# Performance work log

Hardware: AMD Instinct MI355X
Metric: run time of the kernel (lower is better)

Reference implementation:

```python
import jax, jax.numpy as jnp
import numpy as np

B, SEQ, H = 256, 200, 256
NFFT, HOP = 16, 8
FREQ = NFFT // 2 + 1          # 9
NSEG = SEQ // HOP + 1         # 26 (SEQ % HOP == 0 -> pad_len == 0)
FACTOR = 2


def _gelu(x):
    return jax.nn.gelu(x, approximate=False)  # torch nn.GELU / F.gelu default = exact erf


def _layernorm(x, w, b, eps=1e-12):
    u = x.mean(-1, keepdims=True)
    s = ((x - u) ** 2).mean(-1, keepdims=True)
    return w * (x - u) / jnp.sqrt(s + eps) + b


def _mixer(xr, xi, w1, b1, w2, b2):
    # complex MLP: einsum '...ijk,jkl->...ijl' with per-kept-dim weights
    e = lambda a, w: jnp.einsum('bijk,jkl->bijl', a, w)
    o1r = _gelu(e(xr, w1[0]) - e(xi, w1[1]) + b1[0])
    o1i = _gelu(e(xi, w1[0]) + e(xr, w1[1]) + b1[1])
    o2r = e(o1r, w2[0]) - e(o1i, w2[1]) + b2[0]
    # NOTE: faithful to the source bug: o1_image used in BOTH terms of o2_image
    o2i = e(o1i, w2[0]) + e(o1i, w2[1]) + b2[1]
    return o2r, o2i


def _stft(x):
    # torch.stft(n_fft=NFFT, hop=HOP, center=True, onesided=True, normalized=True,
    #            pad_mode='constant', window=None -> rectangular ones)
    pad = NFFT // 2
    xp = jnp.pad(x, ((0, 0), (pad, pad)))
    idx = jnp.arange(NSEG)[:, None] * HOP + jnp.arange(NFFT)[None, :]
    frames = xp[:, idx]                                    # [N, NSEG, NFFT]
    spec = jnp.fft.rfft(frames, axis=-1) * (NFFT ** -0.5)  # normalized=True
    return jnp.swapaxes(spec, -1, -2)                      # [N, FREQ, NSEG]


def _istft(spec):
    # torch.istft(center=True, normalized=True, rectangular window)
    n = spec.shape[0]
    frames = jnp.fft.irfft(jnp.swapaxes(spec, -1, -2) * (NFFT ** 0.5), n=NFFT, axis=-1)
    L = (NSEG - 1) * HOP + NFFT
    idx = (jnp.arange(NSEG)[:, None] * HOP + jnp.arange(NFFT)[None, :]).ravel()
    y = jnp.zeros((n, L), frames.dtype).at[:, idx].add(frames.reshape(n, -1))
    env = jnp.zeros((L,), frames.dtype).at[idx].add(1.0)   # window**2 overlap-add
    pad = NFFT // 2
    out_len = (NSEG - 1) * HOP                              # = SEQ
    return y[:, pad:pad + out_len] / env[pad:pad + out_len]


def setup_inputs() -> dict:
    key = jax.random.key(0)
    ks = jax.random.split(key, 24)
    p = lambda k, sh: jax.random.normal(k, sh, jnp.float32) * 0.02
    d = {}
    d["input_tensor"] = jax.random.normal(ks[0], (B, SEQ, H), jnp.float32)
    # grouped conv2d: weight [NSEG, 1, H, FREQ] -> stored as [NSEG, H, FREQ]
    d["conv_w"] = p(ks[1], (NSEG, H, FREQ)); d["conv_b"] = p(ks[2], (NSEG,))
    d["fm_w1"] = p(ks[3], (2, NSEG, FREQ, FREQ * FACTOR)); d["fm_b1"] = p(ks[4], (2, NSEG, FREQ * FACTOR))
    d["fm_w2"] = p(ks[5], (2, NSEG, FREQ * FACTOR, FREQ)); d["fm_b2"] = p(ks[6], (2, NSEG, FREQ))
    d["cm_w1"] = p(ks[7], (2, NSEG, H, H * FACTOR)); d["cm_b1"] = p(ks[8], (2, NSEG, H * FACTOR))
    d["cm_w2"] = p(ks[9], (2, NSEG, H * FACTOR, H)); d["cm_b2"] = p(ks[10], (2, NSEG, H))
    d["sm_w1"] = p(ks[11], (2, FREQ, NSEG, NSEG * FACTOR)); d["sm_b1"] = p(ks[12], (2, FREQ, NSEG * FACTOR))
    d["sm_w2"] = p(ks[13], (2, FREQ, NSEG * FACTOR, NSEG)); d["sm_b2"] = p(ks[14], (2, FREQ, NSEG))
    d["ln_w"] = jnp.ones((H,), jnp.float32); d["ln_b"] = jnp.zeros((H,), jnp.float32)
    d["ff_w1"] = p(ks[15], (H, 4 * H)); d["ff_b1"] = p(ks[16], (4 * H,))
    d["ff_w2"] = p(ks[17], (4 * H, H)); d["ff_b2"] = p(ks[18], (H,))
    d["ff_ln_w"] = jnp.ones((H,), jnp.float32); d["ff_ln_b"] = jnp.zeros((H,), jnp.float32)
    return d


def reference(input_tensor, conv_w, conv_b, fm_w1, fm_b1, fm_w2, fm_b2,
              cm_w1, cm_b1, cm_w2, cm_b2, sm_w1, sm_b1, sm_w2, sm_b2,
              ln_w, ln_b, ff_w1, ff_b1, ff_w2, ff_b2, ff_ln_w, ff_ln_b):
    b, seq, h = input_tensor.shape
    x = jnp.swapaxes(input_tensor, -1, -2).reshape(b * h, seq)  # pad_len == 0
    spec = _stft(x).reshape(b, h, FREQ, NSEG)
    xr, xi = spec.real, spec.imag
    xnorm = jnp.sqrt(xr ** 2 + xi ** 2)                         # [b,h,F,S]
    # grouped conv2d with full (H,FREQ) kernel == per-segment weighted sum
    w = jnp.einsum('bhfs,shf->bs', xnorm, conv_w) + conv_b
    w = w + jnp.exp(jnp.arange(1 - NSEG, 1, dtype=jnp.float32))  # exp decay bias
    xr = xr * w[:, None, None, :]
    xi = xi * w[:, None, None, :]
    # -> [b,h,S,F]: frequency mixing (kept=segment, mixed=freq)
    xr = jnp.swapaxes(xr, -1, -2); xi = jnp.swapaxes(xi, -1, -2)
    xr, xi = _mixer(xr, xi, fm_w1, fm_b1, fm_w2, fm_b2)
    # -> [b,F,S,h]: channel mixing (kept=segment, mixed=hidden)
    xr = jnp.swapaxes(xr, 1, 3); xi = jnp.swapaxes(xi, 1, 3)
    xr, xi = _mixer(xr, xi, cm_w1, cm_b1, cm_w2, cm_b2)
    # -> [b,h,F,S]: segment mixing (kept=freq, mixed=segment)
    xr = jnp.transpose(xr, (0, 3, 1, 2)); xi = jnp.transpose(xi, (0, 3, 1, 2))
    xr, xi = _mixer(xr, xi, sm_w1, sm_b1, sm_w2, sm_b2)
    spec = (xr + 1j * xi).reshape(b * h, FREQ, NSEG)
    y = _istft(spec)[:, :seq].reshape(b, h, seq)
    y = jnp.swapaxes(y, -1, -2)                                  # [b,seq,h]
    hs = _layernorm(y + input_tensor, ln_w, ln_b)                # dropout p=0
    ff = _gelu(hs @ ff_w1 + ff_b1) @ ff_w2 + ff_b2
    return _layernorm(ff + hs, ff_ln_w, ff_ln_b)
```

## Files before the change

kernel.cpp:

```cpp
#include <hip/hip_runtime.h>
#include <hip/hip_bf16.h>
#include <math.h>

typedef __hip_bfloat16 bf16;
typedef short bf16x8 __attribute__((ext_vector_type(8)));
typedef float f32x4 __attribute__((ext_vector_type(4)));

#define B_    256
#define SEQ_  200
#define H_    256
#define FREQ_ 9
#define NSEG_ 26
#define LDS64 64

__device__ __forceinline__ float ldb(const bf16* p, size_t i){ return __bfloat162float(p[i]); }
__device__ __forceinline__ void stb(bf16* p, size_t i, float v){ p[i] = __float2bfloat16(v); }
__device__ __forceinline__ short f2b(float v){ union{bf16 b; short s;} c; c.b = __float2bfloat16(v); return c.s; }
__device__ __forceinline__ unsigned short f2bu(float v){ union{bf16 b; unsigned short s;} c; c.b = __float2bfloat16(v); return c.s; }
__device__ __forceinline__ float gelu_(float x){
  float y  = 0.7978845608f*(x + 0.044715f*x*x*x);
  float ay = fabsf(y);
  float e  = __expf(-2.f*ay);
  float th = 1.f - 2.f*e*__builtin_amdgcn_rcpf(1.f + e);
  th = copysignf(th, y);
  return 0.5f*x*(1.f + th);
}

__device__ __constant__ float CT16[16] = {
  1.0f, 0.9238795325f, 0.7071067812f, 0.3826834324f, 0.0f, -0.3826834324f, -0.7071067812f, -0.9238795325f,
 -1.0f,-0.9238795325f,-0.7071067812f,-0.3826834324f, 0.0f,  0.3826834324f, 0.7071067812f,  0.9238795325f};
__device__ __constant__ float ST16[16] = {
  0.0f, 0.3826834324f, 0.7071067812f, 0.9238795325f, 1.0f,  0.9238795325f, 0.7071067812f,  0.3826834324f,
  0.0f,-0.3826834324f,-0.7071067812f,-0.9238795325f,-1.0f, -0.9238795325f,-0.7071067812f, -0.3826834324f};

__device__ __forceinline__ void gload16(const short* g, short* l){
  __builtin_amdgcn_global_load_lds(
      (const __attribute__((address_space(1))) unsigned int*)(const void*)g,
      (__attribute__((address_space(3))) unsigned int*)(void*)l, 16, 0, 0);
}

template<int ROWS>
__device__ __forceinline__ void stage_tile(short* lds, const short* src, int rstride, int tid){
  int rl = tid >> 3;
  int c  = tid & 7;
  #pragma unroll
  for(int p=0; p<ROWS/32; p++){
    int r = p*32 + rl;
    int csrc = c ^ (r & 7);
    gload16(src + (size_t)r*rstride + csrc*8, lds + r*LDS64 + c*8);
  }
}

__device__ __forceinline__ void mma_bk64(const short* lA, const short* lB, int wm, int wn,
                                         int lane, f32x4 acc[4][4]){
  int m_l = lane & 15, quad = lane >> 4;
  int sw = m_l & 7;
  #pragma unroll
  for(int ks=0; ks<64; ks+=32){
    int cs = (((ks>>3) + quad) ^ sw) * 8;
    bf16x8 a[4], b[4];
    #pragma unroll
    for(int i=0;i<4;i++) a[i] = *(const bf16x8*)&lA[(wm + i*16 + m_l)*LDS64 + cs];
    #pragma unroll
    for(int j=0;j<4;j++) b[j] = *(const bf16x8*)&lB[(wn + j*16 + m_l)*LDS64 + cs];
    #pragma unroll
    for(int i=0;i<4;i++)
      #pragma unroll
      for(int j=0;j<4;j++)
        acc[i][j] = __builtin_amdgcn_mfma_f32_16x16x32_bf16(a[i], b[j], acc[i][j], 0,0,0);
  }
}

__global__ __launch_bounds__(256) void k_prep_b1(const float* __restrict__ w1, short* __restrict__ B1t){
  int g = blockIdx.x;
  int jt = g & 7, ht = (g>>3)&3, p = (g>>5)&1, s = g>>6;
  __shared__ float tile[64][65];
  int t = threadIdx.x;
  const float* src = w1 + (size_t)p*3407872 + (size_t)s*131072;
  #pragma unroll
  for(int q=0;q<16;q++){
    int r = q*4 + (t>>6), c = t & 63;
    tile[r][c] = src[(size_t)(ht*64 + r)*512 + jt*64 + c];
  }
  __syncthreads();
  int n_l = t >> 2, kc = (t & 3)*16;
  short tA[16] __attribute__((aligned(16)));
  short tB[16] __attribute__((aligned(16)));
  #pragma unroll
  for(int i=0;i<16;i++){
    float v = tile[kc+i][n_l];
    tA[i] = (p==0) ? f2b(v) : f2b(-v);
    tB[i] = f2b(v);
  }
  int j = jt*64 + n_l, h = ht*64 + kc;
  size_t d1, d2;
  if(p==0){ d1 = ((size_t)(s*1024 + j))*512 + h;
            d2 = ((size_t)(s*1024 + 512 + j))*512 + 256 + h; }
  else    { d1 = ((size_t)(s*1024 + j))*512 + 256 + h;
            d2 = ((size_t)(s*1024 + 512 + j))*512 + h; }
  *(int4*)&B1t[d1] = *(int4*)&tA[0]; *(int4*)&B1t[d1+8] = *(int4*)&tA[8];
  *(int4*)&B1t[d2] = *(int4*)&tB[0]; *(int4*)&B1t[d2+8] = *(int4*)&tB[8];
}

__global__ __launch_bounds__(256) void k_prep_b2(const float* __restrict__ w2,
                                                 short* __restrict__ B2r, short* __restrict__ B2i){
  int g = blockIdx.x;
  int ht = g & 3, jt = (g>>2)&7, s = g>>5;
  __shared__ float t0[64][65], t1[64][65];
  int t = threadIdx.x;
  const float* s0 = w2 + (size_t)s*131072;
  const float* s1 = w2 + 3407872 + (size_t)s*131072;
  #pragma unroll
  for(int q=0;q<16;q++){
    int r = q*4 + (t>>6), c = t & 63;
    t0[r][c] = s0[(size_t)(jt*64 + r)*256 + ht*64 + c];
    t1[r][c] = s1[(size_t)(jt*64 + r)*256 + ht*64 + c];
  }
  __syncthreads();
  int n_l = t >> 2, jc = (t & 3)*16;
  short ta[16] __attribute__((aligned(16)));
  short tb[16] __attribute__((aligned(16)));
  short tc[16] __attribute__((aligned(16)));
  #pragma unroll
  for(int i=0;i<16;i++){
    float v0 = t0[jc+i][n_l], v1 = t1[jc+i][n_l];
    ta[i] = f2b(v0); tb[i] = f2b(-v1); tc[i] = f2b(v0+v1);
  }
  int n = ht*64 + n_l, j = jt*64 + jc;
  size_t dr = ((size_t)(s*256 + n))*1024 + j;
  size_t di = ((size_t)(s*256 + n))*512 + j;
  *(int4*)&B2r[dr]     = *(int4*)&ta[0]; *(int4*)&B2r[dr+8]     = *(int4*)&ta[8];
  *(int4*)&B2r[dr+512] = *(int4*)&tb[0]; *(int4*)&B2r[dr+520]   = *(int4*)&tb[8];
  *(int4*)&B2i[di]     = *(int4*)&tc[0]; *(int4*)&B2i[di+8]     = *(int4*)&tc[8];
}

__global__ __launch_bounds__(256) void k_transp(const float* __restrict__ src, short* __restrict__ dst,
                                                int R, int C){
  int ct = blockIdx.x % (C/64);
  int rt = blockIdx.x / (C/64);
  __shared__ float tile[64][65];
  int t = threadIdx.x;
  #pragma unroll
  for(int p=0;p<16;p++){
    int r = p*4 + (t>>6), c = t & 63;
    tile[r][c] = src[(size_t)(rt*64 + r)*C + ct*64 + c];
  }
  __syncthreads();
  int row_out = t >> 2, rc = (t & 3)*16;
  short tmp[16] __attribute__((aligned(16)));
  #pragma unroll
  for(int i=0;i<16;i++) tmp[i] = f2b(tile[rc+i][row_out]);
  size_t base = (size_t)(ct*64 + row_out)*R + rt*64 + rc;
  *(int4*)&dst[base] = *(int4*)&tmp[0]; *(int4*)&dst[base+8] = *(int4*)&tmp[8];
}

__global__ __launch_bounds__(256) void k_prep_sm(const float* __restrict__ w1, const float* __restrict__ w2,
                                                 short* __restrict__ B1sm, short* __restrict__ B2sm){
  int f = blockIdx.x;
  int t = threadIdx.x;
  for(int idx=t; idx<8192; idx+=256){
    int jp = idx >> 6, k = idx & 63;
    float v = 0.f;
    if(jp < 104){
      int j = (jp < 52) ? jp : jp - 52;
      if(k < 26){
        int s = k;
        v = (jp < 52) ? w1[f*1352 + s*52 + j] : w1[12168 + f*1352 + s*52 + j];
      } else if(k >= 32 && k < 58){
        int s = k - 32;
        v = (jp < 52) ? -w1[12168 + f*1352 + s*52 + j] : w1[f*1352 + s*52 + j];
      }
    }
    B1sm[(size_t)f*8192 + idx] = f2b(v);
  }
  for(int idx=t; idx<8192; idx+=256){
    int sop = idx >> 7, k = idx & 127;
    float v = 0.f;
    if(sop < 26){
      if(k < 52)       v = w2[f*1352 + k*26 + sop];
      else if(k < 104) v = -w2[12168 + f*1352 + (k-52)*26 + sop];
    } else if(sop < 52){
      int so = sop - 26;
      if(k >= 52 && k < 104)
        v = w2[f*1352 + (k-52)*26 + so] + w2[12168 + f*1352 + (k-52)*26 + so];
    }
    B2sm[(size_t)f*8192 + idx] = f2b(v);
  }
}

__global__ __launch_bounds__(256) void k_prep_fm(const float* __restrict__ w1, const float* __restrict__ w2,
                                                 short* __restrict__ B1fm, short* __restrict__ B2fm){
  int s = blockIdx.x;
  int t = threadIdx.x;
  for(int idx=t; idx<1536; idx+=256){
    int n = idx >> 5, k = idx & 31;
    float v = 0.f;
    if(n < 18){
      if(k < 9)       v = w1[s*162 + k*18 + n];
      else if(k < 18) v = -w1[4212 + s*162 + (k-9)*18 + n];
    } else if(n < 36){
      int j = n - 18;
      if(k < 9)       v = w1[4212 + s*162 + k*18 + j];
      else if(k < 18) v = w1[s*162 + (k-9)*18 + j];
    }
    B1fm[s*1536 + idx] = f2b(v);
  }
  for(int idx=t; idx<2048; idx+=256){
    int n = idx >> 6, k = idx & 63;
    float v = 0.f;
    if(n < 9){
      if(k < 18)      v = w2[s*162 + k*9 + n];
      else if(k < 36) v = -w2[4212 + s*162 + (k-18)*9 + n];
    } else if(n < 18){
      int f = n - 9;
      if(k >= 18 && k < 36)
        v = w2[s*162 + (k-18)*9 + f] + w2[4212 + s*162 + (k-18)*9 + f];
    }
    B2fm[s*2048 + idx] = f2b(v);
  }
}

__global__ __launch_bounds__(256) void k_prep_cw(const float* __restrict__ cw, float* __restrict__ cwT){
  int s = blockIdx.x; int t = threadIdx.x;
  __shared__ float tile[2304];
  for(int i=t; i<2304; i+=256) tile[i] = cw[s*2304 + i];
  __syncthreads();
  #pragma unroll
  for(int f=0; f<9; f++) cwT[(s*9+f)*256 + t] = tile[t*9+f];
}

#define LX1 40
#define LG1 72
__global__ __launch_bounds__(256) void k_sfm2(const float* __restrict__ inp,
                                              const float* __restrict__ cwT, const float* __restrict__ cb,
                                              const short* __restrict__ B1fm, const short* __restrict__ B2fm,
                                              const float* __restrict__ bb1, const float* __restrict__ bb2,
                                              bf16* __restrict__ oR, bf16* __restrict__ oI){
  int blk = blockIdx.x; int b = blk / NSEG_; int s = blk % NSEG_; int t = threadIdx.x;
  int lane = t & 63, wave = t >> 6, m_l = lane & 15, quad = lane >> 4;
  __shared__ __align__(16) short sm[20736];
  __shared__ float wred[4];
  __shared__ float lb1f[48];
  short* lX  = sm;
  short* lB1 = sm + 10240;
  short* lG  = sm;
  short* lB2 = sm + 18432;

  {
    const short* src1 = B1fm + s*1536;
    for(int idx=t; idx<768; idx+=256){
      int r = idx >> 4, c = idx & 15;
      *(unsigned*)&lB1[r*LX1 + c*2] = *(const unsigned*)&src1[r*32 + c*2];
    }
    const short* src2 = B2fm + s*2048;
    for(int idx=t; idx<1024; idx+=256){
      int r = idx >> 5, c = idx & 31;
      *(unsigned*)&lB2[r*LG1 + c*2] = *(const unsigned*)&src2[r*64 + c*2];
    }
    if(t < 48) lb1f[t] = (t < 18) ? bb1[s*18 + t] : (t < 36 ? bb1[468 + s*18 + (t-18)] : 0.f);
  }

  float cwv[9];
  #pragma unroll
  for(int f=0;f<9;f++) cwv[f] = cwT[(s*9+f)*256 + t];

  float xv[16];
  int t0 = s*8 - 8;
  #pragma unroll
  for(int k=0;k<16;k++){
    int tt = t0 + k;
    xv[k] = (tt>=0 && tt<SEQ_) ? inp[(size_t)(b*SEQ_+tt)*H_ + t] : 0.0f;
  }
  float xr[9], xi[9];
  float acc = 0.f;
  #pragma unroll
  for(int f=0;f<FREQ_;f++){
    float ar=0.f, ai=0.f;
    #pragma unroll
    for(int k=0;k<16;k++){
      int m = (f*k) & 15;
      ar += xv[k]*CT16[m];
      ai -= xv[k]*ST16[m];
    }
    xr[f] = 0.25f*ar; xi[f] = 0.25f*ai;
    acc += sqrtf(xr[f]*xr[f] + xi[f]*xi[f]) * cwv[f];
  }

  #pragma unroll
  for(int msk=1; msk<64; msk<<=1) acc += __shfl_xor(acc, msk);
  if(lane == 0) wred[wave] = acc;
  __syncthreads();
  float wv = wred[0]+wred[1]+wred[2]+wred[3] + cb[s] + __expf((float)(s - (NSEG_-1)));

  {
    float vb[32];
    #pragma unroll
    for(int f=0;f<9;f++){ vb[f] = xr[f]*wv; vb[9+f] = xi[f]*wv; }
    #pragma unroll
    for(int k=18;k<32;k++) vb[k] = 0.f;
    union { unsigned u[16]; int4 v4[4]; } pk;
    #pragma unroll
    for(int c=0;c<16;c++)
      pk.u[c] = (unsigned)f2bu(vb[2*c]) | ((unsigned)f2bu(vb[2*c+1]) << 16);
    #pragma unroll
    for(int q=0;q<4;q++) *(int4*)&lX[t*LX1 + q*8] = pk.v4[q];
  }
  __syncthreads();

  int h0 = wave*64;
  f32x4 acc1[4][3];
  #pragma unroll
  for(int i=0;i<4;i++)
    #pragma unroll
    for(int j=0;j<3;j++) acc1[i][j] = (f32x4){0.f,0.f,0.f,0.f};
  {
    bf16x8 a1[4], b1v[3];
    #pragma unroll
    for(int i=0;i<4;i++) a1[i] = *(const bf16x8*)&lX[(h0 + i*16 + m_l)*LX1 + quad*8];
    #pragma unroll
    for(int j=0;j<3;j++) b1v[j] = *(const bf16x8*)&lB1[(j*16 + m_l)*LX1 + quad*8];
    #pragma unroll
    for(int i=0;i<4;i++)
      #pragma unroll
      for(int j=0;j<3;j++)
        acc1[i][j] = __builtin_amdgcn_mfma_f32_16x16x32_bf16(a1[i], b1v[j], acc1[i][j], 0,0,0);
  }
  __syncthreads();

  #pragma unroll
  for(int i=0;i<4;i++){
    #pragma unroll
    for(int j=0;j<3;j++){
      int n = j*16 + m_l;
      float bias = lb1f[n];
      #pragma unroll
      for(int r=0;r<4;r++){
        int row = h0 + i*16 + quad*4 + r;
        lG[row*LG1 + n] = f2b(gelu_(acc1[i][j][r] + bias));
      }
    }
  }
  #pragma unroll
  for(int c=0;c<8;c++) *(unsigned*)&lG[t*LG1 + 48 + c*2] = 0u;
  __syncthreads();

  f32x4 acc2[4][2];
  #pragma unroll
  for(int i=0;i<4;i++)
    #pragma unroll
    for(int j=0;j<2;j++) acc2[i][j] = (f32x4){0.f,0.f,0.f,0.f};
  #pragma unroll
  for(int ks=0; ks<64; ks+=32){
    bf16x8 a2[4], b2v[2];
    #pragma unroll
    for(int i=0;i<4;i++) a2[i] = *(const bf16x8*)&lG[(h0 + i*16 + m_l)*LG1 + ks + quad*8];
    #pragma unroll
    for(int j=0;j<2;j++) b2v[j] = *(const bf16x8*)&lB2[(j*16 + m_l)*LG1 + ks + quad*8];
    #pragma unroll
    for(int i=0;i<4;i++)
      #pragma unroll
      for(int j=0;j<2;j++)
        acc2[i][j] = __builtin_amdgcn_mfma_f32_16x16x32_bf16(a2[i], b2v[j], acc2[i][j], 0,0,0);
  }

  #pragma unroll
  for(int j=0;j<2;j++){
    int n = j*16 + m_l;
    if(n < 18){
      bool isI = n >= 9;
      int f = isI ? n-9 : n;
      float bias = isI ? bb2[234 + s*9 + f] : bb2[s*9 + f];
      bf16* outp = isI ? oI : oR;
      size_t base = ((size_t)(s*B_ + b)*FREQ_ + f)*H_;
      #pragma unroll
      for(int i=0;i<4;i++){
        int h = h0 + i*16 + quad*4;
        short pk[4] __attribute__((aligned(8)));
        #pragma unroll
        for(int r=0;r<4;r++) pk[r] = f2b(acc2[i][j][r] + bias);
        *(int2*)&outp[base + h] = *(const int2*)&pk[0];
      }
    }
  }
}

__global__ __launch_bounds__(256) void k_cm1(const bf16* __restrict__ Xr, const bf16* __restrict__ Xi,
                                             const short* __restrict__ B1t, const float* __restrict__ b1bias,
                                             short* __restrict__ H, int half){
  int nt = blockIdx.x & 7, mt = (blockIdx.x >> 3) % 9, s = blockIdx.x / 72;
  int tid = threadIdx.x, lane = tid & 63, wave = tid >> 6;
  int wm = (wave & 1)*64, wn = (wave >> 1)*64;
  __shared__ __align__(16) short lA[128*LDS64];
  __shared__ __align__(16) short lB[128*LDS64];
  f32x4 acc[4][4];
  #pragma unroll
  for(int i=0;i<4;i++)
    #pragma unroll
    for(int j=0;j<4;j++) acc[i][j] = (f32x4){0.f,0.f,0.f,0.f};
  int rowbase = half*1152 + mt*128;
  const short* Bbase = B1t + ((size_t)(s*1024 + nt*128))*512;
  for(int k0=0; k0<512; k0+=64){
    const short* Asrc = (k0 < 256)
      ? (const short*)(Xr + ((size_t)(s*2304 + rowbase))*256 + k0)
      : (const short*)(Xi + ((size_t)(s*2304 + rowbase))*256 + (k0-256));
    stage_tile<128>(lA, Asrc, 256, tid);
    stage_tile<128>(lB, Bbase + k0, 512, tid);
    __syncthreads();
    mma_bk64(lA, lB, wm, wn, lane, acc);
    __syncthreads();
  }
  int m_l = lane & 15, quad = lane >> 4;
  #pragma unroll
  for(int i=0;i<4;i++){
    #pragma unroll
    for(int j=0;j<4;j++){
      int n = nt*128 + wn + j*16 + m_l;
      float bias = (n < 512) ? b1bias[s*512 + n] : b1bias[13312 + s*512 + (n-512)];
      #pragma unroll
      for(int r=0;r<4;r++){
        int mrow = wm + i*16 + quad*4 + r;
        float v = gelu_(acc[i][j][r] + bias);
        H[((size_t)(s*1152 + mt*128 + mrow))*1024 + n] = f2b(v);
      }
    }
  }
}

__global__ __launch_bounds__(256) void k_cm2(const short* __restrict__ H,
                                             const short* __restrict__ B2r, const short* __restrict__ B2i,
                                             const float* __restrict__ b2bias,
                                             bf16* __restrict__ oR, bf16* __restrict__ oI, int half){
  int nt = blockIdx.x & 3, mt = (blockIdx.x>>2) % 9, s = blockIdx.x / 36;
  int tid = threadIdx.x, lane = tid & 63, wave = tid >> 6;
  int wm = (wave & 1)*64, wn = (wave >> 1)*64;
  bool isOi = nt >= 2;
  int n0 = (nt & 1)*128;
  int K = isOi ? 512 : 1024;
  int Aoff = isOi ? 512 : 0;
  int Bstride = isOi ? 512 : 1024;
  const short* Bb = isOi ? (B2i + ((size_t)(s*256 + n0))*512) : (B2r + ((size_t)(s*256 + n0))*1024);
  const short* Ab = H + ((size_t)(s*1152 + mt*128))*1024 + Aoff;
  __shared__ __align__(16) short lA[128*LDS64];
  __shared__ __align__(16) short lB[128*LDS64];
  f32x4 acc[4][4];
  #pragma unroll
  for(int i=0;i<4;i++)
    #pragma unroll
    for(int j=0;j<4;j++) acc[i][j] = (f32x4){0.f,0.f,0.f,0.f};
  for(int k0=0; k0<K; k0+=64){
    stage_tile<128>(lA, Ab + k0, 1024, tid);
    stage_tile<128>(lB, Bb + k0, Bstride, tid);
    __syncthreads();
    mma_bk64(lA, lB, wm, wn, lane, acc);
    __syncthreads();
  }
  int m_l = lane & 15, quad = lane >> 4;
  bf16* outp = isOi ? oI : oR;
  #pragma unroll
  for(int i=0;i<4;i++){
    #pragma unroll
    for(int j=0;j<4;j++){
      int n = n0 + wn + j*16 + m_l;
      float bias = b2bias[(isOi ? 6656 : 0) + s*256 + n];
      #pragma unroll
      for(int r=0;r<4;r++){
        int mrow = wm + i*16 + quad*4 + r;
        int rowg = half*1152 + mt*128 + mrow;
        stb(outp, ((size_t)rowg*NSEG_ + s)*256 + n, acc[i][j][r] + bias);
      }
    }
  }
}

#define LDX 72
#define LDG 136
__global__ __launch_bounds__(512) void k_smm(const bf16* __restrict__ iR, const bf16* __restrict__ iI,
                                             const short* __restrict__ B1sm, const short* __restrict__ B2sm,
                                             const float* __restrict__ bb1, const float* __restrict__ bb2,
                                             bf16* __restrict__ oR, bf16* __restrict__ oI){
  int blk = blockIdx.x;
  int f  = blk % 9;
  int hh = (blk/9) & 1;
  int bq = blk / 18;
  int t = threadIdx.x, lane = t & 63, wave = t >> 6;
  int m_l = lane & 15, quad = lane >> 4;
  __shared__ __align__(16) short sm[18432 + 8704];
  __shared__ float lb1[128];
  short* lX  = sm;
  short* lB1 = sm + 128*LDX;
  short* lG  = sm;
  short* lB2 = sm + 18432;
  int rbase = (bq*9 + f)*26;

  #pragma unroll
  for(int it=0; it<2; it++){
    int idx = it*512 + t;
    int r = idx >> 3, c = idx & 7;
    *(int4*)&lB1[r*LDX + c*8] = *(const int4*)&B1sm[(size_t)f*8192 + r*64 + c*8];
  }
  #pragma unroll
  for(int it=0; it<2; it++){
    int idx = it*512 + t;
    int r = idx >> 4, c = idx & 15;
    *(int4*)&lB2[r*LDG + c*8] = *(const int4*)&B2sm[(size_t)f*8192 + r*128 + c*8];
  }
  if(t < 128) lb1[t] = (t < 52) ? bb1[f*52 + t] : (t < 104 ? bb1[468 + f*52 + (t-52)] : 0.f);

  int hl = t & 127, g = t >> 7;
  #pragma unroll
  for(int it=0; it<7; it++){
    int a = it*4 + g;
    if(a < 26){
      int arr = a >= 13;
      int pr  = arr ? a-13 : a;
      int s0  = pr*2;
      const bf16* src = arr ? iI : iR;
      unsigned v0 = *(const unsigned short*)&src[((size_t)(rbase+s0  ))*256 + hh*128 + hl];
      unsigned v1 = *(const unsigned short*)&src[((size_t)(rbase+s0+1))*256 + hh*128 + hl];
      *(unsigned*)&lX[hl*LDX + arr*32 + s0] = v0 | (v1 << 16);
    }
  }
  if(g < 2){
    int zb = g ? 58 : 26;
    #pragma unroll
    for(int i=0;i<3;i++) *(unsigned*)&lX[hl*LDX + zb + i*2] = 0u;
  }
  __syncthreads();

  int h0 = wave*16;
  f32x4 acc1[8];
  #pragma unroll
  for(int j=0;j<8;j++) acc1[j] = (f32x4){0.f,0.f,0.f,0.f};
  #pragma unroll
  for(int ks=0; ks<64; ks+=32){
    bf16x8 av, bv[8];
    av = *(const bf16x8*)&lX[(h0 + m_l)*LDX + ks + quad*8];
    #pragma unroll
    for(int j=0;j<8;j++) bv[j] = *(const bf16x8*)&lB1[(j*16 + m_l)*LDX + ks + quad*8];
    #pragma unroll
    for(int j=0;j<8;j++)
      acc1[j] = __builtin_amdgcn_mfma_f32_16x16x32_bf16(av, bv[j], acc1[j], 0,0,0);
  }
  __syncthreads();

  #pragma unroll
  for(int j=0;j<8;j++){
    int jp = j*16 + m_l;
    float bias = lb1[jp];
    #pragma unroll
    for(int r=0;r<4;r++){
      int hrow = h0 + quad*4 + r;
      lG[hrow*LDG + jp] = f2b(gelu_(acc1[j][r] + bias));
    }
  }
  __syncthreads();

  f32x4 acc2[4];
  #pragma unroll
  for(int j=0;j<4;j++) acc2[j] = (f32x4){0.f,0.f,0.f,0.f};
  #pragma unroll
  for(int ks=0; ks<128; ks+=32){
    bf16x8 av, bv[4];
    av = *(const bf16x8*)&lG[(h0 + m_l)*LDG + ks + quad*8];
    #pragma unroll
    for(int j=0;j<4;j++) bv[j] = *(const bf16x8*)&lB2[(j*16 + m_l)*LDG + ks + quad*8];
    #pragma unroll
    for(int j=0;j<4;j++)
      acc2[j] = __builtin_amdgcn_mfma_f32_16x16x32_bf16(av, bv[j], acc2[j], 0,0,0);
  }

  #pragma unroll
  for(int j=0;j<4;j++){
    int sop = j*16 + m_l;
    if(sop < 52){
      int arr = sop >= 26;
      int so  = sop - (arr ? 26 : 0);
      float bias = bb2[(arr ? 234 : 0) + f*26 + so];
      bf16* outp = arr ? oI : oR;
      int h = hh*128 + h0 + quad*4;
      short pk[4] __attribute__((aligned(8)));
      #pragma unroll
      for(int r=0;r<4;r++) pk[r] = f2b(acc2[j][r] + bias);
      *(int2*)&outp[((size_t)(rbase + so))*256 + h] = *(const int2*)&pk[0];
    }
  }
}

__global__ __launch_bounds__(256) void k_ist8(const bf16* __restrict__ iR, const bf16* __restrict__ iI,
                                              const float* __restrict__ inp,
                                              const float* __restrict__ lnw, const float* __restrict__ lnb,
                                              float* __restrict__ hs, bf16* __restrict__ hsb){
  int blk = blockIdx.x; int b = blk / 25; int o = blk % 25; int h = threadIdx.x;
  int lane = h & 63, wave = h >> 6;
  float rr[2][9], ii[2][8];
  #pragma unroll
  for(int p=0;p<2;p++){
    int s = o + p;
    size_t base = (size_t)b*FREQ_*NSEG_ + s;
    #pragma unroll
    for(int f=0;f<9;f++) rr[p][f] = ldb(iR, (base + f*NSEG_)*256 + h);
    #pragma unroll
    for(int f=1;f<8;f++) ii[p][f] = ldb(iI, (base + f*NSEG_)*256 + h);
  }
  float z[8];
  #pragma unroll
  for(int dt=0; dt<8; dt++){
    float v  = rr[0][0] + rr[1][0];
    float s8 = rr[0][8] + rr[1][8];
    v += (dt & 1) ? -s8 : s8;
    #pragma unroll
    for(int f=1;f<8;f++){
      int m1 = (f*(dt+8)) & 15;
      int m2 = (f*dt) & 15;
      v += 2.f*(rr[0][f]*CT16[m1] - ii[0][f]*ST16[m1]);
      v += 2.f*(rr[1][f]*CT16[m2] - ii[1][f]*ST16[m2]);
    }
    int t = o*8 + dt;
    z[dt] = 0.125f*v + inp[(size_t)(b*SEQ_+t)*H_ + h];
  }
  __shared__ float wsum[8][4], wsq[8][4];
  #pragma unroll
  for(int dt=0; dt<8; dt++){
    float sv = z[dt], sq = z[dt]*z[dt];
    #pragma unroll
    for(int msk=1; msk<64; msk<<=1){ sv += __shfl_xor(sv, msk); sq += __shfl_xor(sq, msk); }
    if(lane == 0){ wsum[dt][wave] = sv; wsq[dt][wave] = sq; }
  }
  __syncthreads();
  float gw = lnw[h], gb = lnb[h];
  #pragma unroll
  for(int dt=0; dt<8; dt++){
    float s1 = wsum[dt][0]+wsum[dt][1]+wsum[dt][2]+wsum[dt][3];
    float s2 = wsq[dt][0]+wsq[dt][1]+wsq[dt][2]+wsq[dt][3];
    float mean = s1*(1.f/256.f);
    float var  = s2*(1.f/256.f) - mean*mean;
    float inv  = rsqrtf(var + 1e-12f);
    float ov = gw*(z[dt]-mean)*inv + gb;
    int t = o*8 + dt;
    size_t oi = (size_t)(b*SEQ_+t)*H_ + h;
    hs[oi] = ov;
    stb(hsb, oi, ov);
  }
}

__global__ __launch_bounds__(256) void k_ff1m(const short* __restrict__ hsb, const short* __restrict__ fw1t,
                                              const float* __restrict__ fb1, short* __restrict__ hid, int row0){
  int nt = blockIdx.x & 7, mt = blockIdx.x >> 3;
  int tid = threadIdx.x, lane = tid & 63, wave = tid >> 6;
  int wm = (wave & 1)*64, wn = (wave >> 1)*64;
  __shared__ __align__(16) short lA[128*LDS64];
  __shared__ __align__(16) short lB[128*LDS64];
  f32x4 acc[4][4];
  #pragma unroll
  for(int i=0;i<4;i++)
    #pragma unroll
    for(int j=0;j<4;j++) acc[i][j] = (f32x4){0.f,0.f,0.f,0.f};
  const short* Ab = hsb + ((size_t)(row0 + mt*128))*256;
  const short* Bb = fw1t + ((size_t)(nt*128))*256;
  for(int k0=0; k0<256; k0+=64){
    stage_tile<128>(lA, Ab + k0, 256, tid);
    stage_tile<128>(lB, Bb + k0, 256, tid);
    __syncthreads();
    mma_bk64(lA, lB, wm, wn, lane, acc);
    __syncthreads();
  }
  int m_l = lane & 15, quad = lane >> 4;
  #pragma unroll
  for(int i=0;i<4;i++){
    #pragma unroll
    for(int j=0;j<4;j++){
      int n = nt*128 + wn + j*16 + m_l;
      float bias = fb1[n];
      #pragma unroll
      for(int r=0;r<4;r++){
        int mrow = wm + i*16 + quad*4 + r;
        hid[((size_t)(mt*128 + mrow))*1024 + n] = f2b(gelu_(acc[i][j][r] + bias));
      }
    }
  }
}

__global__ __launch_bounds__(256) void k_ff2m(const short* __restrict__ hid, const short* __restrict__ fw2t,
                                              const float* __restrict__ fb2, const float* __restrict__ hs,
                                              const float* __restrict__ lnw, const float* __restrict__ lnb,
                                              float* __restrict__ out, int row0){
  int mt = blockIdx.x;
  int tid = threadIdx.x, lane = tid & 63, wave = tid >> 6;
  int wn = wave*64;
  __shared__ __align__(16) short lA[64*LDS64];
  __shared__ __align__(16) short lB[256*LDS64];
  __shared__ float ssum[64][4], ssq[64][4];
  f32x4 acc[4][4];
  #pragma unroll
  for(int i=0;i<4;i++)
    #pragma unroll
    for(int j=0;j<4;j++) acc[i][j] = (f32x4){0.f,0.f,0.f,0.f};
  const short* Ab = hid + ((size_t)(mt*64))*1024;
  for(int k0=0; k0<1024; k0+=64){
    stage_tile<64>(lA, Ab + k0, 1024, tid);
    stage_tile<256>(lB, fw2t + k0, 1024, tid);
    __syncthreads();
    mma_bk64(lA, lB, 0, wn, lane, acc);
    __syncthreads();
  }
  int m_l = lane & 15, quad = lane >> 4;
  int rowg0 = row0 + mt*64;
  #pragma unroll
  for(int i=0;i<4;i++){
    #pragma unroll
    for(int j=0;j<4;j++){
      int col = wn + j*16 + m_l;
      float bias = fb2[col];
      #pragma unroll
      for(int r=0;r<4;r++){
        int mrow = i*16 + quad*4 + r;
        acc[i][j][r] += bias + hs[(size_t)(rowg0+mrow)*256 + col];
      }
    }
  }
  #pragma unroll
  for(int i=0;i<4;i++){
    #pragma unroll
    for(int r=0;r<4;r++){
      float sv = 0.f, sq = 0.f;
      #pragma unroll
      for(int j=0;j<4;j++){ float v = acc[i][j][r]; sv += v; sq += v*v; }
      #pragma unroll
      for(int msk=1; msk<16; msk<<=1){ sv += __shfl_xor(sv, msk); sq += __shfl_xor(sq, msk); }
      if(m_l == 0){ int mrow = i*16 + quad*4 + r; ssum[mrow][wave] = sv; ssq[mrow][wave] = sq; }
    }
  }
  __syncthreads();
  if(tid < 64){
    float s1 = ssum[tid][0]+ssum[tid][1]+ssum[tid][2]+ssum[tid][3];
    float s2 = ssq[tid][0]+ssq[tid][1]+ssq[tid][2]+ssq[tid][3];
    float mean = s1*(1.f/256.f);
    float var  = s2*(1.f/256.f) - mean*mean;
    ssum[tid][0] = mean;
    ssq[tid][0]  = rsqrtf(var + 1e-12f);
  }
  __syncthreads();
  #pragma unroll
  for(int i=0;i<4;i++){
    #pragma unroll
    for(int j=0;j<4;j++){
      int col = wn + j*16 + m_l;
      float gw = lnw[col], gb = lnb[col];
      #pragma unroll
      for(int r=0;r<4;r++){
        int mrow = i*16 + quad*4 + r;
        float mean = ssum[mrow][0], inv = ssq[mrow][0];
        out[(size_t)(rowg0+mrow)*256 + col] = (acc[i][j][r] - mean)*inv*gw + gb;
      }
    }
  }
}

extern "C" void kernel_launch(void* const* d_in, const int* in_sizes, int n_in,
                              void* d_out, int out_size, void* d_ws, size_t ws_size,
                              hipStream_t stream){
  const float* inp    = (const float*)d_in[0];
  const float* conv_w = (const float*)d_in[1];
  const float* conv_b = (const float*)d_in[2];
  const float* fm_w1  = (const float*)d_in[3];
  const float* fm_b1  = (const float*)d_in[4];
  const float* fm_w2  = (const float*)d_in[5];
  const float* fm_b2  = (const float*)d_in[6];
  const float* cm_w1  = (const float*)d_in[7];
  const float* cm_b1  = (const float*)d_in[8];
  const float* cm_w2  = (const float*)d_in[9];
  const float* cm_b2  = (const float*)d_in[10];
  const float* sm_w1  = (const float*)d_in[11];
  const float* sm_b1  = (const float*)d_in[12];
  const float* sm_w2  = (const float*)d_in[13];
  const float* sm_b2  = (const float*)d_in[14];
  const float* ln_w   = (const float*)d_in[15];
  const float* ln_b   = (const float*)d_in[16];
  const float* ff_w1  = (const float*)d_in[17];
  const float* ff_b1  = (const float*)d_in[18];
  const float* ff_w2  = (const float*)d_in[19];
  const float* ff_b2  = (const float*)d_in[20];
  const float* ffln_w = (const float*)d_in[21];
  const float* ffln_b = (const float*)d_in[22];
  float* out = (float*)d_out;

  const size_t NS = (size_t)B_ * NSEG_ * FREQ_ * H_;
  const size_t HN = (size_t)NSEG_ * 1152 * 1024;
  short* ws = (short*)d_ws;
  bf16*  b0   = (bf16*)ws;
  bf16*  b1   = (bf16*)(ws + NS);
  bf16*  b2   = (bf16*)(ws + 2*NS);
  bf16*  b3   = (bf16*)(ws + 3*NS);
  short* H    = ws + 4*NS;
  short* B1t  = H + HN;
  short* B2r  = B1t + (size_t)26*1024*512;
  short* B2i  = B2r + (size_t)26*256*1024;
  short* fw1t = B2i + (size_t)26*256*512;
  short* fw2t = fw1t + 262144;
  short* B1sm = fw2t + 262144;
  short* B2sm = B1sm + 73728;
  short* B1fm = B2sm + 73728;
  short* B2fm = B1fm + 39936;
  float* cwT  = (float*)(B2fm + 53248);
  float* hs   = (float*)b0;
  bf16*  hsb  = (bf16*)H;
  short* hid  = (short*)b2;

  k_prep_b1<<<1664, 256, 0, stream>>>(cm_w1, B1t);
  k_prep_b2<<<832,  256, 0, stream>>>(cm_w2, B2r, B2i);
  k_transp <<<64,   256, 0, stream>>>(ff_w1, fw1t, 256, 1024);
  k_transp <<<64,   256, 0, stream>>>(ff_w2, fw2t, 1024, 256);
  k_prep_sm<<<9,    256, 0, stream>>>(sm_w1, sm_w2, B1sm, B2sm);
  k_prep_fm<<<26,   256, 0, stream>>>(fm_w1, fm_w2, B1fm, B2fm);
  k_prep_cw<<<26,   256, 0, stream>>>(conv_w, cwT);

  k_sfm2<<<B_*NSEG_, 256, 0, stream>>>(inp, cwT, conv_b, B1fm, B2fm, fm_b1, fm_b2, b2, b3);
  for(int half=0; half<2; half++){
    k_cm1<<<26*72, 256, 0, stream>>>(b2, b3, B1t, cm_b1, H, half);
    k_cm2<<<26*36, 256, 0, stream>>>(H, B2r, B2i, cm_b2, b0, b1, half);
  }
  k_smm<<<B_*2*FREQ_, 512, 0, stream>>>(b0, b1, B1sm, B2sm, sm_b1, sm_b2, b2, b3);
  k_ist8<<<B_*25, 256, 0, stream>>>(b2, b3, inp, ln_w, ln_b, hs, hsb);
  for(int c=0; c<2; c++){
    int row0 = c*25600;
    k_ff1m<<<1600, 256, 0, stream>>>((const short*)hsb, fw1t, ff_b1, hid, row0);
    k_ff2m<<<400,  256, 0, stream>>>(hid, fw2t, ff_b2, hs, ffln_w, ffln_b, out, row0);
  }
}
```

Before: 839.1 us.

## Process four batches per segment-mixer block with register prefetch of next input

```diff
diff --git a/kernel.cpp b/kernel.cpp
--- a/kernel.cpp
+++ b/kernel.cpp
@@ -474,14 +474,15 @@
 
 #define LDX 72
 #define LDG 136
-__global__ __launch_bounds__(512) void k_smm(const bf16* __restrict__ iR, const bf16* __restrict__ iI,
-                                             const short* __restrict__ B1sm, const short* __restrict__ B2sm,
-                                             const float* __restrict__ bb1, const float* __restrict__ bb2,
-                                             bf16* __restrict__ oR, bf16* __restrict__ oI){
+#define NT_ 4
+__global__ __launch_bounds__(512) void k_smm4(const bf16* __restrict__ iR, const bf16* __restrict__ iI,
+                                              const short* __restrict__ B1sm, const short* __restrict__ B2sm,
+                                              const float* __restrict__ bb1, const float* __restrict__ bb2,
+                                              bf16* __restrict__ oR, bf16* __restrict__ oI){
   int blk = blockIdx.x;
   int f  = blk % 9;
   int hh = (blk/9) & 1;
-  int bq = blk / 18;
+  int bq0 = (blk/18)*NT_;
   int t = threadIdx.x, lane = t & 63, wave = t >> 6;
   int m_l = lane & 15, quad = lane >> 4;
   __shared__ __align__(16) short sm[18432 + 8704];
@@ -490,98 +491,152 @@
   short* lB1 = sm + 128*LDX;
   short* lG  = sm;
   short* lB2 = sm + 18432;
-  int rbase = (bq*9 + f)*26;
-
-  #pragma unroll
-  for(int it=0; it<2; it++){
-    int idx = it*512 + t;
-    int r = idx >> 3, c = idx & 7;
-    *(int4*)&lB1[r*LDX + c*8] = *(const int4*)&B1sm[(size_t)f*8192 + r*64 + c*8];
-  }
-  #pragma unroll
-  for(int it=0; it<2; it++){
-    int idx = it*512 + t;
-    int r = idx >> 4, c = idx & 15;
-    *(int4*)&lB2[r*LDG + c*8] = *(const int4*)&B2sm[(size_t)f*8192 + r*128 + c*8];
-  }
-  if(t < 128) lb1[t] = (t < 52) ? bb1[f*52 + t] : (t < 104 ? bb1[468 + f*52 + (t-52)] : 0.f);
+
+  int4 pb[2];
+  {
+    #pragma unroll
+    for(int it=0; it<2; it++){
+      int idx = it*512 + t;
+      int r = idx >> 3, c = idx & 7;
+      pb[it] = *(const int4*)&B1sm[(size_t)f*8192 + r*64 + c*8];
+      *(int4*)&lB1[r*LDX + c*8] = pb[it];
+    }
+    #pragma unroll
+    for(int it=0; it<2; it++){
+      int idx = it*512 + t;
+      int r = idx >> 4, c = idx & 15;
+      *(int4*)&lB2[r*LDG + c*8] = *(const int4*)&B2sm[(size_t)f*8192 + r*128 + c*8];
+    }
+    if(t < 128) lb1[t] = (t < 52) ? bb1[f*52 + t] : (t < 104 ? bb1[468 + f*52 + (t-52)] : 0.f);
+  }
 
   int hl = t & 127, g = t >> 7;
-  #pragma unroll
-  for(int it=0; it<7; it++){
-    int a = it*4 + g;
-    if(a < 26){
-      int arr = a >= 13;
-      int pr  = arr ? a-13 : a;
-      int s0  = pr*2;
-      const bf16* src = arr ? iI : iR;
-      unsigned v0 = *(const unsigned short*)&src[((size_t)(rbase+s0  ))*256 + hh*128 + hl];
-      unsigned v1 = *(const unsigned short*)&src[((size_t)(rbase+s0+1))*256 + hh*128 + hl];
-      *(unsigned*)&lX[hl*LDX + arr*32 + s0] = v0 | (v1 << 16);
-    }
-  }
-  if(g < 2){
-    int zb = g ? 58 : 26;
-    #pragma unroll
-    for(int i=0;i<3;i++) *(unsigned*)&lX[hl*LDX + zb + i*2] = 0u;
+  {
+    int rb = (bq0*9 + f)*26;
+    #pragma unroll
+    for(int it=0; it<7; it++){
+      int a = it*4 + g;
+      if(a < 26){
+        int arr = a >= 13;
+        int pr  = arr ? a-13 : a;
+        int s0  = pr*2;
+        const bf16* src = arr ? iI : iR;
+        unsigned v0 = *(const unsigned short*)&src[((size_t)(rb+s0  ))*256 + hh*128 + hl];
+        unsigned v1 = *(const unsigned short*)&src[((size_t)(rb+s0+1))*256 + hh*128 + hl];
+        *(unsigned*)&lX[hl*LDX + arr*32 + s0] = v0 | (v1 << 16);
+      }
+    }
+    if(g < 2){
+      int zb = g ? 58 : 26;
+      #pragma unroll
+      for(int i=0;i<3;i++) *(unsigned*)&lX[hl*LDX + zb + i*2] = 0u;
+    }
   }
   __syncthreads();
 
   int h0 = wave*16;
-  f32x4 acc1[8];
-  #pragma unroll
-  for(int j=0;j<8;j++) acc1[j] = (f32x4){0.f,0.f,0.f,0.f};
-  #pragma unroll
-  for(int ks=0; ks<64; ks+=32){
-    bf16x8 av, bv[8];
-    av = *(const bf16x8*)&lX[(h0 + m_l)*LDX + ks + quad*8];
-    #pragma unroll
-    for(int j=0;j<8;j++) bv[j] = *(const bf16x8*)&lB1[(j*16 + m_l)*LDX + ks + quad*8];
-    #pragma unroll
-    for(int j=0;j<8;j++)
-      acc1[j] = __builtin_amdgcn_mfma_f32_16x16x32_bf16(av, bv[j], acc1[j], 0,0,0);
-  }
-  __syncthreads();
-
-  #pragma unroll
-  for(int j=0;j<8;j++){
-    int jp = j*16 + m_l;
-    float bias = lb1[jp];
-    #pragma unroll
-    for(int r=0;r<4;r++){
-      int hrow = h0 + quad*4 + r;
-      lG[hrow*LDG + jp] = f2b(gelu_(acc1[j][r] + bias));
-    }
-  }
-  __syncthreads();
-
-  f32x4 acc2[4];
-  #pragma unroll
-  for(int j=0;j<4;j++) acc2[j] = (f32x4){0.f,0.f,0.f,0.f};
-  #pragma unroll
-  for(int ks=0; ks<128; ks+=32){
-    bf16x8 av, bv[4];
-    av = *(const bf16x8*)&lG[(h0 + m_l)*LDG + ks + quad*8];
-    #pragma unroll
-    for(int j=0;j<4;j++) bv[j] = *(const bf16x8*)&lB2[(j*16 + m_l)*LDG + ks + quad*8];
-    #pragma unroll
-    for(int j=0;j<4;j++)
-      acc2[j] = __builtin_amdgcn_mfma_f32_16x16x32_bf16(av, bv[j], acc2[j], 0,0,0);
-  }
-
-  #pragma unroll
-  for(int j=0;j<4;j++){
-    int sop = j*16 + m_l;
-    if(sop < 52){
-      int arr = sop >= 26;
-      int so  = sop - (arr ? 26 : 0);
-      float bias = bb2[(arr ? 234 : 0) + f*26 + so];
-      bf16* outp = arr ? oI : oR;
-      int h = hh*128 + h0 + quad*4;
-      short pk[4] __attribute__((aligned(8)));
-      #pragma unroll
-      for(int r=0;r<4;r++) pk[r] = f2b(acc2[j][r] + bias);
-      *(int2*)&outp[((size_t)(rbase + so))*256 + h] = *(const int2*)&pk[0];
+  for(int nt=0; nt<NT_; nt++){
+    int bq = bq0 + nt;
+    int rbase = (bq*9 + f)*26;
+    bool havep = (nt+1 < NT_);
+
+    f32x4 acc1[8];
+    #pragma unroll
+    for(int j=0;j<8;j++) acc1[j] = (f32x4){0.f,0.f,0.f,0.f};
+    #pragma unroll
+    for(int ks=0; ks<64; ks+=32){
+      bf16x8 av = *(const bf16x8*)&lX[(h0 + m_l)*LDX + ks + quad*8];
+      bf16x8 bv[8];
+      #pragma unroll
+      for(int j=0;j<8;j++) bv[j] = *(const bf16x8*)&lB1[(j*16 + m_l)*LDX + ks + quad*8];
+      #pragma unroll
+      for(int j=0;j<8;j++)
+        acc1[j] = __builtin_amdgcn_mfma_f32_16x16x32_bf16(av, bv[j], acc1[j], 0,0,0);
+    }
+    __syncthreads();
+
+    unsigned px[7];
+    if(havep){
+      int rb = ((bq+1)*9 + f)*26;
+      #pragma unroll
+      for(int it=0; it<7; it++){
+        int a = it*4 + g;
+        if(a < 26){
+          int arr = a >= 13;
+          int pr  = arr ? a-13 : a;
+          int s0  = pr*2;
+          const bf16* src = arr ? iI : iR;
+          unsigned v0 = *(const unsigned short*)&src[((size_t)(rb+s0  ))*256 + hh*128 + hl];
+          unsigned v1 = *(const unsigned short*)&src[((size_t)(rb+s0+1))*256 + hh*128 + hl];
+          px[it] = v0 | (v1 << 16);
+        }
+      }
+    }
+
+    #pragma unroll
+    for(int j=0;j<8;j++){
+      int jp = j*16 + m_l;
+      float bias = lb1[jp];
+      #pragma unroll
+      for(int r=0;r<4;r++){
+        int hrow = h0 + quad*4 + r;
+        lG[hrow*LDG + jp] = f2b(gelu_(acc1[j][r] + bias));
+      }
+    }
+    __syncthreads();
+
+    f32x4 acc2[4];
+    #pragma unroll
+    for(int j=0;j<4;j++) acc2[j] = (f32x4){0.f,0.f,0.f,0.f};
+    #pragma unroll
+    for(int ks=0; ks<128; ks+=32){
+      bf16x8 av = *(const bf16x8*)&lG[(h0 + m_l)*LDG + ks + quad*8];
+      bf16x8 bv[4];
+      #pragma unroll
+      for(int j=0;j<4;j++) bv[j] = *(const bf16x8*)&lB2[(j*16 + m_l)*LDG + ks + quad*8];
+      #pragma unroll
+      for(int j=0;j<4;j++)
+        acc2[j] = __builtin_amdgcn_mfma_f32_16x16x32_bf16(av, bv[j], acc2[j], 0,0,0);
+    }
+    #pragma unroll
+    for(int j=0;j<4;j++){
+      int sop = j*16 + m_l;
+      if(sop < 52){
+        int arr = sop >= 26;
+        int so  = sop - (arr ? 26 : 0);
+        float bias = bb2[(arr ? 234 : 0) + f*26 + so];
+        bf16* outp = arr ? oI : oR;
+        int h = hh*128 + h0 + quad*4;
+        short pk[4] __attribute__((aligned(8)));
+        #pragma unroll
+        for(int r=0;r<4;r++) pk[r] = f2b(acc2[j][r] + bias);
+        *(int2*)&outp[((size_t)(rbase + so))*256 + h] = *(const int2*)&pk[0];
+      }
+    }
+
+    if(havep){
+      __syncthreads();
+      #pragma unroll
+      for(int it=0; it<7; it++){
+        int a = it*4 + g;
+        if(a < 26){
+          int arr = a >= 13;
+          int s0 = (arr ? a-13 : a)*2;
+          *(unsigned*)&lX[hl*LDX + arr*32 + s0] = px[it];
+        }
+      }
+      if(g < 2){
+        int zb = g ? 58 : 26;
+        #pragma unroll
+        for(int i=0;i<3;i++) *(unsigned*)&lX[hl*LDX + zb + i*2] = 0u;
+      }
+      #pragma unroll
+      for(int it=0; it<2; it++){
+        int idx = it*512 + t;
+        int r = idx >> 3, c = idx & 7;
+        *(int4*)&lB1[r*LDX + c*8] = pb[it];
+      }
+      __syncthreads();
     }
   }
 }
@@ -819,7 +874,7 @@
     k_cm1<<<26*72, 256, 0, stream>>>(b2, b3, B1t, cm_b1, H, half);
     k_cm2<<<26*36, 256, 0, stream>>>(H, B2r, B2i, cm_b2, b0, b1, half);
   }
-  k_smm<<<B_*2*FREQ_, 512, 0, stream>>>(b0, b1, B1sm, B2sm, sm_b1, sm_b2, b2, b3);
+  k_smm4<<<(B_/NT_)*2*FREQ_, 512, 0, stream>>>(b0, b1, B1sm, B2sm, sm_b1, sm_b2, b2, b3);
   k_ist8<<<B_*25, 256, 0, stream>>>(b2, b3, inp, ln_w, ln_b, hs, hsb);
   for(int c=0; c<2; c++){
     int row0 = c*25600;
```

After: 867.4 us. 3.4% more time.
